# Performance work log

Measured on AMD Instinct MI355X. Metric: run time of the kernel, lower is better.

## Reference

```python
import jax, jax.numpy as jnp
import numpy as np

ALPHA = 0.01
EPS = ALPHA / (1.0 - 2.0 * ALPHA)  # boundary_eps


def setup_inputs() -> dict:
    key = jax.random.key(0)
    ks = jax.random.split(key, 9)
    B, D, K = 32768, 256, 1024
    x = jax.random.normal(ks[0], (B, D), dtype=jnp.float32)
    logp = jnp.zeros((B, 1), dtype=jnp.float32)
    actnorm1_bias = jax.random.normal(ks[1], (D,), dtype=jnp.float32) * 0.1
    actnorm1_weight = jax.random.normal(ks[2], (D,), dtype=jnp.float32) * 0.1
    actnorm2_bias = jax.random.normal(ks[3], (D,), dtype=jnp.float32) * 0.1
    actnorm2_weight = jax.random.normal(ks[4], (D,), dtype=jnp.float32) * 0.1
    shift_coeff = jax.random.normal(ks[5], (D,), dtype=jnp.float32)
    anchor_pts = jax.random.normal(ks[6], (K, D), dtype=jnp.float32)
    mixture_logits = jax.random.normal(ks[7], (K,), dtype=jnp.float32) * 0.1
    u = jax.random.uniform(ks[8], (D,), dtype=jnp.float32)
    box_min = -(u + 1.0) * 2.0  # guarantees box_max > box_min
    box_max = (u + 1.0) * 2.0
    return dict(x=x, logp=logp, actnorm1_bias=actnorm1_bias,
                actnorm1_weight=actnorm1_weight, actnorm2_bias=actnorm2_bias,
                actnorm2_weight=actnorm2_weight, shift_coeff=shift_coeff,
                anchor_pts=anchor_pts, mixture_logits=mixture_logits,
                box_min=box_min, box_max=box_max)


def _voronoi_forward(x, logp, a1b, a1w, a2b, a2w, shift_raw, anchors, mix_logits,
                     box_min, box_max):
    B, D = x.shape
    # actnorm1: y = (x + bias) * exp(weight); logp -= logdet
    x = (x + a1b) * jnp.exp(a1w)
    logp = logp - jnp.sum(a1w)
    # logit_transform.inverse: x = (sigmoid(x) - alpha) / (1 - 2*alpha)
    s = jax.nn.sigmoid(x)
    logdet = jnp.sum(jax.nn.log_sigmoid(x) + jax.nn.log_sigmoid(-x)
                     - jnp.log(1.0 - 2.0 * ALPHA), axis=1, keepdims=True)
    x = (s - ALPHA) / (1.0 - 2.0 * ALPHA)
    logp = logp - logdet
    # rescale from [-eps, 1+eps] to [0, 1]
    lo, hi = -EPS, 1.0 + EPS
    x = (x - lo) / (hi - lo)
    logp = logp - (-jnp.log(hi - lo) * D)
    # box constraints: affine to [box_min, box_max]
    x = x * (box_max - box_min) + box_min
    logp = logp - jnp.sum(jnp.log(box_max - box_min))
    # find_nearest: argmin squared distance over K anchors (GEMM form, no BxKxD tensor)
    d2 = (jnp.sum(x * x, axis=1, keepdims=True)
          - 2.0 * x @ anchors.T
          + jnp.sum(anchors * anchors, axis=1))  # [B, K]
    idx = jnp.argmin(d2, axis=1)  # [B]
    x_k = anchors[idx]  # gather nearest anchor, [B, D]
    # shift toward the nearest anchor
    sc = jax.nn.sigmoid(shift_raw) * 0.98 + 0.01  # (0.01, 0.99)
    x = x + sc * (x_k - x)
    logp = logp - jnp.sum(jnp.log(1.0 - sc))
    # map_outside_cell: identity with zero logdet (see notes)
    # recentre on the chosen anchor
    x = x - x_k
    # actnorm2
    x = (x + a2b) * jnp.exp(a2w)
    logp = logp - jnp.sum(a2w)
    # mixture log-prob gather
    logp_k = jax.nn.log_softmax(mix_logits)[idx][:, None]
    logp = logp - logp_k
    return x, logp, idx


def reference(x, logp, actnorm1_bias, actnorm1_weight, actnorm2_bias,
              actnorm2_weight, shift_coeff, anchor_pts, mixture_logits,
              box_min, box_max):
    return _voronoi_forward(x, logp, actnorm1_bias, actnorm1_weight,
                            actnorm2_bias, actnorm2_weight, shift_coeff,
                            anchor_pts, mixture_logits, box_min, box_max)
```

## Files before the change

### kernel.cpp

```cpp
#include <hip/hip_runtime.h>
#include <math.h>

namespace {
constexpr int Brows = 32768;
constexpr int Dd = 256;
constexpr int Kk = 1024;

constexpr double kAlpha64 = 0.01;
constexpr double kC164 = 1.0 - 2.0 * 0.01;
constexpr double kEps64 = 0.01 / (1.0 - 2.0 * 0.01);
constexpr double kLo64 = -kEps64;
constexpr double kHi64 = 1.0 + kEps64;

constexpr int WS_E1W = 0;
constexpr int WS_WD = 256;
constexpr int WS_P = 512;
constexpr int WS_Q = 768;
constexpr int WS_C = 1024;
constexpr int WS_AA = 1088;
constexpr int WS_LSM = 2112;
}

__global__ void precol_kernel(const float* __restrict__ a1w,
                              const float* __restrict__ a2w,
                              const float* __restrict__ a2b,
                              const float* __restrict__ shiftc,
                              const float* __restrict__ bmin,
                              const float* __restrict__ bmax,
                              float* __restrict__ ws) {
  const int d = threadIdx.x;
  const float w1 = a1w[d], w2 = a2w[d];
  const float wd = __fsub_rn(bmax[d], bmin[d]);
  const float sc = 1.0f / (1.0f + expf(-shiftc[d])) * 0.98f + 0.01f;
  const float e2 = expf(w2);
  ws[WS_E1W + d] = expf(w1);
  ws[WS_WD + d] = wd;
  ws[WS_P + d] = (1.0f - sc) * e2;
  ws[WS_Q + d] = a2b[d] * e2;
  float contrib = -w1 - w2 - logf(wd) - logf(1.0f - sc);
#pragma unroll
  for (int o = 32; o > 0; o >>= 1) contrib += __shfl_xor(contrib, o, 64);
  __shared__ float red[4];
  if ((d & 63) == 0) red[d >> 6] = contrib;
  __syncthreads();
  if (d == 0) {
    float Cv = red[0] + red[1] + red[2] + red[3];
    Cv += (float)Dd * (float)(log(kC164) + log(kHi64 - kLo64));
    ws[WS_C] = Cv;
  }
}

template <typename F>
__device__ inline float pw128_sq(F ld) {
  float r[8];
#pragma unroll
  for (int j = 0; j < 8; ++j) {
    const float v = ld(j);
    r[j] = __fmul_rn(v, v);
  }
  for (int i = 8; i < 128; i += 8) {
#pragma unroll
    for (int j = 0; j < 8; ++j) {
      const float v = ld(i + j);
      r[j] = __fadd_rn(r[j], __fmul_rn(v, v));
    }
  }
  const float s01 = __fadd_rn(r[0], r[1]);
  const float s23 = __fadd_rn(r[2], r[3]);
  const float s45 = __fadd_rn(r[4], r[5]);
  const float s67 = __fadd_rn(r[6], r[7]);
  return __fadd_rn(__fadd_rn(s01, s23), __fadd_rn(s45, s67));
}

__global__ void anorm_kernel(const float* __restrict__ anchors,
                             float* __restrict__ ws) {
  const int k = blockIdx.x * 256 + threadIdx.x;
  const float* a = anchors + (size_t)k * Dd;
  const float b0 = pw128_sq([&](int i) { return a[i]; });
  const float b1 = pw128_sq([&](int i) { return a[128 + i]; });
  ws[WS_AA + k] = __fadd_rn(b0, b1);
}

__global__ void lsm_kernel(const float* __restrict__ logits,
                           float* __restrict__ ws) {
  __shared__ float sm[1024];
  const int t = threadIdx.x;
  const float v = logits[t];
  sm[t] = v;
  __syncthreads();
  for (int o = 512; o > 0; o >>= 1) {
    if (t < o) sm[t] = fmaxf(sm[t], sm[t + o]);
    __syncthreads();
  }
  const float mx = sm[0];
  __syncthreads();
  sm[t] = expf(v - mx);
  __syncthreads();
  for (int o = 512; o > 0; o >>= 1) {
    if (t < o) sm[t] += sm[t + o];
    __syncthreads();
  }
  const float lse = mx + logf(sm[0]);
  ws[WS_LSM + t] = v - lse;
}

__global__ __launch_bounds__(256, 2) void voronoi_main(
    const float* __restrict__ x, const float* __restrict__ logp_in,
    const float* __restrict__ a1b, const float* __restrict__ anchors,
    const float* __restrict__ bmin, const float* __restrict__ ws,
    float* __restrict__ out) {
  __shared__ float xt[Dd][68];
  __shared__ float at[8][256];
  __shared__ float logdet_s[64];
  __shared__ float xx_s[64];
  __shared__ int bidx_s[64];

  const int t = threadIdx.x;
  const int r0 = blockIdx.x * 64;

  const float LOF = (float)kLo64;
  const float HLF = (float)(kHi64 - kLo64);
  const float ALPHAF = (float)kAlpha64;
  const float C1F = (float)kC164;

  {
    const int r = t >> 2, j = t & 3;
    const float* xrow = x + (size_t)(r0 + r) * Dd;
    float ld = 0.0f;
#pragma unroll
    for (int it = 0; it < 16; ++it) {
      const int c = it * 16 + j * 4;
      const float4 xv = *(const float4*)(xrow + c);
      const float4 bv = *(const float4*)(a1b + c);
      const float4 ev = *(const float4*)(ws + WS_E1W + c);
      const float4 wv = *(const float4*)(ws + WS_WD + c);
      const float4 mv = *(const float4*)(bmin + c);
      const float xs[4] = {xv.x, xv.y, xv.z, xv.w};
      const float bs[4] = {bv.x, bv.y, bv.z, bv.w};
      const float es[4] = {ev.x, ev.y, ev.z, ev.w};
      const float wds[4] = {wv.x, wv.y, wv.z, wv.w};
      const float ms[4] = {mv.x, mv.y, mv.z, mv.w};
#pragma unroll
      for (int w = 0; w < 4; ++w) {
        const float y = __fmul_rn(__fadd_rn(xs[w], bs[w]), es[w]);
        const float ay = fabsf(y);
        const float e = expf(-ay);
        ld += -ay - 2.0f * log1pf(e);
        const float den = __fadd_rn(1.0f, e);
        const float s = (y >= 0.0f) ? __fdiv_rn(1.0f, den) : __fdiv_rn(e, den);
        const float x3 = __fdiv_rn(__fsub_rn(s, ALPHAF), C1F);
        const float x4v = __fdiv_rn(__fsub_rn(x3, LOF), HLF);
        const float x5 = __fadd_rn(__fmul_rn(x4v, wds[w]), ms[w]);
        xt[c + w][r] = x5;
      }
    }
    ld += __shfl_xor(ld, 1, 64);
    ld += __shfl_xor(ld, 2, 64);
    if (j == 0) logdet_s[r] = ld;
  }
  __syncthreads();

  if (t < 64) {
    const float b0 = pw128_sq([&](int i) { return xt[i][t]; });
    const float b1 = pw128_sq([&](int i) { return xt[128 + i][t]; });
    xx_s[t] = __fadd_rn(b0, b1);
  }
  __syncthreads();

  const int tc = t & 63;
  const int tr = t >> 6;
  const int tr16 = tr * 16, tc4 = tc * 4;

  float xxr[16];
#pragma unroll
  for (int i = 0; i < 16; ++i) xxr[i] = xx_s[tr16 + i];

  float bd2[16];
  int bidx[16];
#pragma unroll
  for (int i = 0; i < 16; ++i) {
    bd2[i] = 3.0e38f;
    bidx[i] = 0;
  }

  for (int kt = 0; kt < 4; ++kt) {
    float acc[16][4];
#pragma unroll
    for (int i = 0; i < 16; ++i)
#pragma unroll
      for (int j = 0; j < 4; ++j) acc[i][j] = 0.0f;

    for (int dc = 0; dc < 32; ++dc) {
      __syncthreads();
#pragma unroll
      for (int m = 0; m < 2; ++m) {
        const int u = t + m * 256;
        const int k = u >> 1, q = u & 1;
        const float4 av = *(const float4*)(anchors +
                                           (size_t)(kt * 256 + k) * Dd +
                                           dc * 8 + q * 4);
        at[q * 4 + 0][k] = av.x;
        at[q * 4 + 1][k] = av.y;
        at[q * 4 + 2][k] = av.z;
        at[q * 4 + 3][k] = av.w;
      }
      __syncthreads();
#pragma unroll
      for (int dd = 0; dd < 8; ++dd) {
        const int dg = dc * 8 + dd;
        const float4 xf0 = *(const float4*)(&xt[dg][tr16]);
        const float4 xf1 = *(const float4*)(&xt[dg][tr16 + 4]);
        const float4 xf2 = *(const float4*)(&xt[dg][tr16 + 8]);
        const float4 xf3 = *(const float4*)(&xt[dg][tr16 + 12]);
        const float4 af = *(const float4*)(&at[dd][tc4]);
        const float xv[16] = {xf0.x, xf0.y, xf0.z, xf0.w, xf1.x, xf1.y,
                              xf1.z, xf1.w, xf2.x, xf2.y, xf2.z, xf2.w,
                              xf3.x, xf3.y, xf3.z, xf3.w};
#pragma unroll
        for (int i = 0; i < 16; ++i) {
          acc[i][0] = fmaf(xv[i], af.x, acc[i][0]);
          acc[i][1] = fmaf(xv[i], af.y, acc[i][1]);
          acc[i][2] = fmaf(xv[i], af.z, acc[i][2]);
          acc[i][3] = fmaf(xv[i], af.w, acc[i][3]);
        }
      }
    }
#pragma unroll
    for (int j = 0; j < 4; ++j) {
      const int k = kt * 256 + tc4 + j;
      const float aa = ws[WS_AA + k];
#pragma unroll
      for (int i = 0; i < 16; ++i) {
        const float twod = __fadd_rn(acc[i][j], acc[i][j]);
        const float d2 = __fadd_rn(__fsub_rn(xxr[i], twod), aa);
        if (d2 < bd2[i]) {
          bd2[i] = d2;
          bidx[i] = k;
        }
      }
    }
  }
#pragma unroll
  for (int o = 1; o < 64; o <<= 1) {
#pragma unroll
    for (int i = 0; i < 16; ++i) {
      const float od = __shfl_xor(bd2[i], o, 64);
      const int oi = __shfl_xor(bidx[i], o, 64);
      if (od < bd2[i] || (od == bd2[i] && oi < bidx[i])) {
        bd2[i] = od;
        bidx[i] = oi;
      }
    }
  }
  if (tc == 0) {
#pragma unroll
    for (int i = 0; i < 16; ++i) bidx_s[tr16 + i] = bidx[i];
  }
  __syncthreads();

  {
    const int r = t >> 2, j = t & 3;
    const int k = bidx_s[r];
    const float* arow = anchors + (size_t)k * Dd;
    float* orow = out + (size_t)(r0 + r) * Dd;
#pragma unroll
    for (int it = 0; it < 16; ++it) {
      const int c = it * 16 + j * 4;
      const float4 av = *(const float4*)(arow + c);
      const float4 pv = *(const float4*)(ws + WS_P + c);
      const float4 qv = *(const float4*)(ws + WS_Q + c);
      float4 ov;
      ov.x = fmaf(xt[c + 0][r] - av.x, pv.x, qv.x);
      ov.y = fmaf(xt[c + 1][r] - av.y, pv.y, qv.y);
      ov.z = fmaf(xt[c + 2][r] - av.z, pv.z, qv.z);
      ov.w = fmaf(xt[c + 3][r] - av.w, pv.w, qv.w);
      *(float4*)(orow + c) = ov;
    }
  }
  if (t < 64) {
    const int rr = t;
    const int kk2 = bidx_s[rr];
    const float lp =
        logp_in[r0 + rr] + ws[WS_C] - logdet_s[rr] - ws[WS_LSM + kk2];
    out[(size_t)Brows * Dd + r0 + rr] = lp;
    out[(size_t)Brows * Dd + Brows + r0 + rr] = (float)kk2;
  }
}

extern "C" void kernel_launch(void* const* d_in, const int* in_sizes, int n_in,
                              void* d_out, int out_size, void* d_ws,
                              size_t ws_size, hipStream_t stream) {
  const float* x = (const float*)d_in[0];
  const float* logp = (const float*)d_in[1];
  const float* a1b = (const float*)d_in[2];
  const float* a1w = (const float*)d_in[3];
  const float* a2b = (const float*)d_in[4];
  const float* a2w = (const float*)d_in[5];
  const float* shiftc = (const float*)d_in[6];
  const float* anch = (const float*)d_in[7];
  const float* mixl = (const float*)d_in[8];
  const float* bmin = (const float*)d_in[9];
  const float* bmax = (const float*)d_in[10];
  float* ws = (float*)d_ws;
  float* out = (float*)d_out;

  precol_kernel<<<1, 256, 0, stream>>>(a1w, a2w, a2b, shiftc, bmin, bmax, ws);
  anorm_kernel<<<Kk / 256, 256, 0, stream>>>(anch, ws);
  lsm_kernel<<<1, 1024, 0, stream>>>(mixl, ws);
  voronoi_main<<<Brows / 64, 256, 0, stream>>>(x, logp, a1b, anch, bmin, ws,
                                               out);
}
```

Baseline: 379.9 us.

## Split transform into separate kernel and double-buffer anchor tiles in GEMM kernel

Moves the elementwise sigmoid/box transform into its own kernel that writes a transposed x5 matrix, row norms and logdet to workspace. A new 512-thread GEMM kernel processes 128 rows per block, reads x directly from global memory in the transposed layout, and double-buffers anchor tiles in shared memory so the next tile's load overlaps with compute. This aims to cut per-block shared memory and the serialised transform phase to raise occupancy and overlap. In exchange it adds a 32 MB round trip through global memory, uncached-in-LDS x reads in the inner loop, and depends on the workspace being large enough, with the old kernel kept as a fallback.

```diff
diff --git a/kernel.cpp b/kernel.cpp
--- a/kernel.cpp
+++ b/kernel.cpp
@@ -19,6 +19,10 @@
 constexpr int WS_C = 1024;
 constexpr int WS_AA = 1088;
 constexpr int WS_LSM = 2112;
+constexpr int WS_XX = 4096;
+constexpr int WS_LOGDET = 36864;
+constexpr int WS_X5T = 69632;
+constexpr size_t WS_NEED_BYTES = (size_t)(WS_X5T + Dd * Brows) * 4;
 }
 
 __global__ void precol_kernel(const float* __restrict__ a1w,
@@ -104,7 +108,229 @@
   ws[WS_LSM + t] = v - lse;
 }
 
-__global__ __launch_bounds__(256, 2) void voronoi_main(
+__device__ inline void stage1_transform(const float* __restrict__ x,
+                                        const float* __restrict__ a1b,
+                                        const float* __restrict__ bmin,
+                                        const float* __restrict__ ws,
+                                        float (*xt)[68], int t, int r0,
+                                        float* ld_out ) {
+  const float LOF = (float)kLo64;
+  const float HLF = (float)(kHi64 - kLo64);
+  const float ALPHAF = (float)kAlpha64;
+  const float C1F = (float)kC164;
+  const int r = t >> 2, j = t & 3;
+  const float* xrow = x + (size_t)(r0 + r) * Dd;
+  float ld = 0.0f;
+#pragma unroll
+  for (int it = 0; it < 16; ++it) {
+    const int c = it * 16 + j * 4;
+    const float4 xv = *(const float4*)(xrow + c);
+    const float4 bv = *(const float4*)(a1b + c);
+    const float4 ev = *(const float4*)(ws + WS_E1W + c);
+    const float4 wv = *(const float4*)(ws + WS_WD + c);
+    const float4 mv = *(const float4*)(bmin + c);
+    const float xs[4] = {xv.x, xv.y, xv.z, xv.w};
+    const float bs[4] = {bv.x, bv.y, bv.z, bv.w};
+    const float es[4] = {ev.x, ev.y, ev.z, ev.w};
+    const float wds[4] = {wv.x, wv.y, wv.z, wv.w};
+    const float ms[4] = {mv.x, mv.y, mv.z, mv.w};
+#pragma unroll
+    for (int w = 0; w < 4; ++w) {
+      const float y = __fmul_rn(__fadd_rn(xs[w], bs[w]), es[w]);
+      const float ay = fabsf(y);
+      const float e = expf(-ay);
+      ld += -ay - 2.0f * log1pf(e);
+      const float den = __fadd_rn(1.0f, e);
+      const float s = (y >= 0.0f) ? __fdiv_rn(1.0f, den) : __fdiv_rn(e, den);
+      const float x3 = __fdiv_rn(__fsub_rn(s, ALPHAF), C1F);
+      const float x4v = __fdiv_rn(__fsub_rn(x3, LOF), HLF);
+      const float x5 = __fadd_rn(__fmul_rn(x4v, wds[w]), ms[w]);
+      xt[c + w][r] = x5;
+    }
+  }
+  ld += __shfl_xor(ld, 1, 64);
+  ld += __shfl_xor(ld, 2, 64);
+  *ld_out = ld;
+}
+
+__global__ __launch_bounds__(256, 2) void transform_kernel(
+    const float* __restrict__ x, const float* __restrict__ a1b,
+    const float* __restrict__ bmin, float* __restrict__ ws) {
+  __shared__ float xt[Dd][68];
+  const int t = threadIdx.x;
+  const int r0 = blockIdx.x * 64;
+  float ld;
+  stage1_transform(x, a1b, bmin, ws, xt, t, r0, &ld);
+  if ((t & 3) == 0) ws[WS_LOGDET + r0 + (t >> 2)] = ld;
+  __syncthreads();
+  if (t < 64) {
+    const float b0 = pw128_sq([&](int i) { return xt[i][t]; });
+    const float b1 = pw128_sq([&](int i) { return xt[128 + i][t]; });
+    ws[WS_XX + r0 + t] = __fadd_rn(b0, b1);
+  }
+  const int lane = t & 63, wv = t >> 6;
+#pragma unroll 4
+  for (int i = 0; i < 64; ++i) {
+    const int d = wv + i * 4;
+    ws[WS_X5T + (size_t)d * Brows + r0 + lane] = xt[d][lane];
+  }
+}
+
+__global__ __launch_bounds__(512, 4) void voronoi_gemm(
+    const float* __restrict__ logp_in, const float* __restrict__ anchors,
+    const float* __restrict__ ws, float* __restrict__ out) {
+  __shared__ float at[2][8][256];
+  __shared__ float bd2_s[128];
+  __shared__ int bidx_s[128];
+
+  const int t = threadIdx.x;
+  const int r0 = blockIdx.x * 128;
+  const int tc = t & 63;
+  const int tr = t >> 6;
+  const int tr16 = tr * 16, tc4 = tc * 4;
+  const float* __restrict__ x5t = ws + WS_X5T;
+
+  if (t < 128) {
+    bd2_s[t] = 3.0e38f;
+    bidx_s[t] = 0;
+  }
+
+  const int sk = t >> 1, sh = t & 1;
+
+  for (int kt = 0; kt < 4; ++kt) {
+    float acc[16][4];
+#pragma unroll
+    for (int i = 0; i < 16; ++i)
+#pragma unroll
+      for (int j = 0; j < 4; ++j) acc[i][j] = 0.0f;
+
+    const float* abase =
+        anchors + (size_t)(kt * 256 + sk) * Dd + sh * 4;
+    {
+      const float4 av = *(const float4*)(abase);
+      at[0][sh * 4 + 0][sk] = av.x;
+      at[0][sh * 4 + 1][sk] = av.y;
+      at[0][sh * 4 + 2][sk] = av.z;
+      at[0][sh * 4 + 3][sk] = av.w;
+    }
+    __syncthreads();
+
+    for (int dc = 0; dc < 32; ++dc) {
+      const int buf = dc & 1;
+      float4 avn;
+      if (dc < 31) avn = *(const float4*)(abase + (dc + 1) * 8);
+#pragma unroll
+      for (int dd = 0; dd < 8; ++dd) {
+        const int dg = dc * 8 + dd;
+        const float* xp = x5t + (size_t)dg * Brows + r0 + tr16;
+        const float4 xf0 = *(const float4*)(xp);
+        const float4 xf1 = *(const float4*)(xp + 4);
+        const float4 xf2 = *(const float4*)(xp + 8);
+        const float4 xf3 = *(const float4*)(xp + 12);
+        const float4 af = *(const float4*)(&at[buf][dd][tc4]);
+        const float xv[16] = {xf0.x, xf0.y, xf0.z, xf0.w, xf1.x, xf1.y,
+                              xf1.z, xf1.w, xf2.x, xf2.y, xf2.z, xf2.w,
+                              xf3.x, xf3.y, xf3.z, xf3.w};
+#pragma unroll
+        for (int i = 0; i < 16; ++i) {
+          acc[i][0] = fmaf(xv[i], af.x, acc[i][0]);
+          acc[i][1] = fmaf(xv[i], af.y, acc[i][1]);
+          acc[i][2] = fmaf(xv[i], af.z, acc[i][2]);
+          acc[i][3] = fmaf(xv[i], af.w, acc[i][3]);
+        }
+      }
+      if (dc < 31) {
+        __syncthreads();
+        at[buf ^ 1][sh * 4 + 0][sk] = avn.x;
+        at[buf ^ 1][sh * 4 + 1][sk] = avn.y;
+        at[buf ^ 1][sh * 4 + 2][sk] = avn.z;
+        at[buf ^ 1][sh * 4 + 3][sk] = avn.w;
+        __syncthreads();
+      }
+    }
+
+    float bd2[16];
+    int bidx[16];
+#pragma unroll
+    for (int i = 0; i < 16; ++i) {
+      bd2[i] = 3.0e38f;
+      bidx[i] = 0;
+    }
+#pragma unroll
+    for (int j = 0; j < 4; ++j) {
+      const int k = kt * 256 + tc4 + j;
+      const float aa = ws[WS_AA + k];
+#pragma unroll
+      for (int i = 0; i < 16; ++i) {
+        const float xxv = ws[WS_XX + r0 + tr16 + i];
+        const float twod = __fadd_rn(acc[i][j], acc[i][j]);
+        const float d2 = __fadd_rn(__fsub_rn(xxv, twod), aa);
+        if (d2 < bd2[i]) {
+          bd2[i] = d2;
+          bidx[i] = k;
+        }
+      }
+    }
+#pragma unroll
+    for (int o = 1; o < 64; o <<= 1) {
+#pragma unroll
+      for (int i = 0; i < 16; ++i) {
+        const float od = __shfl_xor(bd2[i], o, 64);
+        const int oi = __shfl_xor(bidx[i], o, 64);
+        if (od < bd2[i] || (od == bd2[i] && oi < bidx[i])) {
+          bd2[i] = od;
+          bidx[i] = oi;
+        }
+      }
+    }
+    if (tc == 0) {
+#pragma unroll
+      for (int i = 0; i < 16; ++i) {
+        const int row = tr16 + i;
+        if (bd2[i] < bd2_s[row] ||
+            (bd2[i] == bd2_s[row] && bidx[i] < bidx_s[row])) {
+          bd2_s[row] = bd2[i];
+          bidx_s[row] = bidx[i];
+        }
+      }
+    }
+    __syncthreads();
+  }
+
+  {
+    const int r = t >> 2, j = t & 3;
+    const int k = bidx_s[r];
+    const float* arow = anchors + (size_t)k * Dd;
+    float* orow = out + (size_t)(r0 + r) * Dd;
+#pragma unroll
+    for (int it = 0; it < 16; ++it) {
+      const int c = it * 16 + j * 4;
+      const float4 av = *(const float4*)(arow + c);
+      const float4 pv = *(const float4*)(ws + WS_P + c);
+      const float4 qv = *(const float4*)(ws + WS_Q + c);
+      float x5v[4];
+#pragma unroll
+      for (int w = 0; w < 4; ++w)
+        x5v[w] = x5t[(size_t)(c + w) * Brows + r0 + r];
+      float4 ov;
+      ov.x = fmaf(x5v[0] - av.x, pv.x, qv.x);
+      ov.y = fmaf(x5v[1] - av.y, pv.y, qv.y);
+      ov.z = fmaf(x5v[2] - av.z, pv.z, qv.z);
+      ov.w = fmaf(x5v[3] - av.w, pv.w, qv.w);
+      *(float4*)(orow + c) = ov;
+    }
+  }
+  if (t < 128) {
+    const int rr = t;
+    const int kk2 = bidx_s[rr];
+    const float lp = logp_in[r0 + rr] + ws[WS_C] -
+                     ws[WS_LOGDET + r0 + rr] - ws[WS_LSM + kk2];
+    out[(size_t)Brows * Dd + r0 + rr] = lp;
+    out[(size_t)Brows * Dd + Brows + r0 + rr] = (float)kk2;
+  }
+}
+
+__global__ __launch_bounds__(256, 2) void voronoi_fb(
     const float* __restrict__ x, const float* __restrict__ logp_in,
     const float* __restrict__ a1b, const float* __restrict__ anchors,
     const float* __restrict__ bmin, const float* __restrict__ ws,
@@ -117,49 +343,10 @@
 
   const int t = threadIdx.x;
   const int r0 = blockIdx.x * 64;
-
-  const float LOF = (float)kLo64;
-  const float HLF = (float)(kHi64 - kLo64);
-  const float ALPHAF = (float)kAlpha64;
-  const float C1F = (float)kC164;
-
-  {
-    const int r = t >> 2, j = t & 3;
-    const float* xrow = x + (size_t)(r0 + r) * Dd;
-    float ld = 0.0f;
-#pragma unroll
-    for (int it = 0; it < 16; ++it) {
-      const int c = it * 16 + j * 4;
-      const float4 xv = *(const float4*)(xrow + c);
-      const float4 bv = *(const float4*)(a1b + c);
-      const float4 ev = *(const float4*)(ws + WS_E1W + c);
-      const float4 wv = *(const float4*)(ws + WS_WD + c);
-      const float4 mv = *(const float4*)(bmin + c);
-      const float xs[4] = {xv.x, xv.y, xv.z, xv.w};
-      const float bs[4] = {bv.x, bv.y, bv.z, bv.w};
-      const float es[4] = {ev.x, ev.y, ev.z, ev.w};
-      const float wds[4] = {wv.x, wv.y, wv.z, wv.w};
-      const float ms[4] = {mv.x, mv.y, mv.z, mv.w};
-#pragma unroll
-      for (int w = 0; w < 4; ++w) {
-        const float y = __fmul_rn(__fadd_rn(xs[w], bs[w]), es[w]);
-        const float ay = fabsf(y);
-        const float e = expf(-ay);
-        ld += -ay - 2.0f * log1pf(e);
-        const float den = __fadd_rn(1.0f, e);
-        const float s = (y >= 0.0f) ? __fdiv_rn(1.0f, den) : __fdiv_rn(e, den);
-        const float x3 = __fdiv_rn(__fsub_rn(s, ALPHAF), C1F);
-        const float x4v = __fdiv_rn(__fsub_rn(x3, LOF), HLF);
-        const float x5 = __fadd_rn(__fmul_rn(x4v, wds[w]), ms[w]);
-        xt[c + w][r] = x5;
-      }
-    }
-    ld += __shfl_xor(ld, 1, 64);
-    ld += __shfl_xor(ld, 2, 64);
-    if (j == 0) logdet_s[r] = ld;
-  }
-  __syncthreads();
-
+  float ld;
+  stage1_transform(x, a1b, bmin, ws, xt, t, r0, &ld);
+  if ((t & 3) == 0) logdet_s[t >> 2] = ld;
+  __syncthreads();
   if (t < 64) {
     const float b0 = pw128_sq([&](int i) { return xt[i][t]; });
     const float b1 = pw128_sq([&](int i) { return xt[128 + i][t]; });
@@ -167,14 +354,11 @@
   }
   __syncthreads();
 
-  const int tc = t & 63;
-  const int tr = t >> 6;
+  const int tc = t & 63, tr = t >> 6;
   const int tr16 = tr * 16, tc4 = tc * 4;
-
   float xxr[16];
 #pragma unroll
   for (int i = 0; i < 16; ++i) xxr[i] = xx_s[tr16 + i];
-
   float bd2[16];
   int bidx[16];
 #pragma unroll
@@ -182,14 +366,12 @@
     bd2[i] = 3.0e38f;
     bidx[i] = 0;
   }
-
   for (int kt = 0; kt < 4; ++kt) {
     float acc[16][4];
 #pragma unroll
     for (int i = 0; i < 16; ++i)
 #pragma unroll
       for (int j = 0; j < 4; ++j) acc[i][j] = 0.0f;
-
     for (int dc = 0; dc < 32; ++dc) {
       __syncthreads();
 #pragma unroll
@@ -257,7 +439,6 @@
     for (int i = 0; i < 16; ++i) bidx_s[tr16 + i] = bidx[i];
   }
   __syncthreads();
-
   {
     const int r = t >> 2, j = t & 3;
     const int k = bidx_s[r];
@@ -307,6 +488,11 @@
   precol_kernel<<<1, 256, 0, stream>>>(a1w, a2w, a2b, shiftc, bmin, bmax, ws);
   anorm_kernel<<<Kk / 256, 256, 0, stream>>>(anch, ws);
   lsm_kernel<<<1, 1024, 0, stream>>>(mixl, ws);
-  voronoi_main<<<Brows / 64, 256, 0, stream>>>(x, logp, a1b, anch, bmin, ws,
+  if (ws_size >= WS_NEED_BYTES) {
+    transform_kernel<<<Brows / 64, 256, 0, stream>>>(x, a1b, bmin, ws);
+    voronoi_gemm<<<Brows / 128, 512, 0, stream>>>(logp, anch, ws, out);
+  } else {
+    voronoi_fb<<<Brows / 64, 256, 0, stream>>>(x, logp, a1b, anch, bmin, ws,
                                                out);
-}
+  }
+}
```

Measured after the change: 1.214 ms. 220% more time.

## Widen per-thread anchor tile to 16x8 with split anchor staging buffers

Applied to the files above, without the earlier changes.

Each thread now accumulates 16 rows by 8 anchors instead of 16 by 4, so the K loop runs 2 passes of 512 anchors instead of 4 passes of 256. Anchors are staged through two 4x256 shared buffers, one float4 per thread per buffer, with an index mapping that gives each thread 8 contiguous anchors. The goal is to load each x value from LDS once per 8 FMAs instead of 4, and to halve the K passes over the x tile. In exchange the accumulators double to 128 registers, which may cause spills or lower occupancy under the (256, 2) launch bounds, and there are twice as many barriers in the D loop.

```diff
diff --git a/kernel.cpp b/kernel.cpp
--- a/kernel.cpp
+++ b/kernel.cpp
@@ -110,7 +110,8 @@
     const float* __restrict__ bmin, const float* __restrict__ ws,
     float* __restrict__ out) {
   __shared__ float xt[Dd][68];
-  __shared__ float at[8][256];
+  __shared__ float bufA[4][256];
+  __shared__ float bufB[4][256];
   __shared__ float logdet_s[64];
   __shared__ float xx_s[64];
   __shared__ int bidx_s[64];
@@ -183,51 +184,62 @@
     bidx[i] = 0;
   }
 
-  for (int kt = 0; kt < 4; ++kt) {
-    float acc[16][4];
+  const int kApre = ((t >> 2) * 8) + (t & 3);
+  const int kBpre = kApre + 4;
+
+  for (int kt = 0; kt < 2; ++kt) {
+    float acc[16][8];
 #pragma unroll
     for (int i = 0; i < 16; ++i)
 #pragma unroll
-      for (int j = 0; j < 4; ++j) acc[i][j] = 0.0f;
-
-    for (int dc = 0; dc < 32; ++dc) {
+      for (int j = 0; j < 8; ++j) acc[i][j] = 0.0f;
+
+    const float* aA = anchors + (size_t)(kt * 512 + kApre) * Dd;
+    const float* aB = anchors + (size_t)(kt * 512 + kBpre) * Dd;
+
+    for (int dc = 0; dc < 64; ++dc) {
       __syncthreads();
-#pragma unroll
-      for (int m = 0; m < 2; ++m) {
-        const int u = t + m * 256;
-        const int k = u >> 1, q = u & 1;
-        const float4 av = *(const float4*)(anchors +
-                                           (size_t)(kt * 256 + k) * Dd +
-                                           dc * 8 + q * 4);
-        at[q * 4 + 0][k] = av.x;
-        at[q * 4 + 1][k] = av.y;
-        at[q * 4 + 2][k] = av.z;
-        at[q * 4 + 3][k] = av.w;
+      {
+        const float4 avA = *(const float4*)(aA + dc * 4);
+        const float4 avB = *(const float4*)(aB + dc * 4);
+        bufA[0][t] = avA.x;
+        bufA[1][t] = avA.y;
+        bufA[2][t] = avA.z;
+        bufA[3][t] = avA.w;
+        bufB[0][t] = avB.x;
+        bufB[1][t] = avB.y;
+        bufB[2][t] = avB.z;
+        bufB[3][t] = avB.w;
       }
       __syncthreads();
 #pragma unroll
-      for (int dd = 0; dd < 8; ++dd) {
-        const int dg = dc * 8 + dd;
+      for (int dd = 0; dd < 4; ++dd) {
+        const int dg = dc * 4 + dd;
         const float4 xf0 = *(const float4*)(&xt[dg][tr16]);
         const float4 xf1 = *(const float4*)(&xt[dg][tr16 + 4]);
         const float4 xf2 = *(const float4*)(&xt[dg][tr16 + 8]);
         const float4 xf3 = *(const float4*)(&xt[dg][tr16 + 12]);
-        const float4 af = *(const float4*)(&at[dd][tc4]);
+        const float4 afA = *(const float4*)(&bufA[dd][tc4]);
+        const float4 afB = *(const float4*)(&bufB[dd][tc4]);
         const float xv[16] = {xf0.x, xf0.y, xf0.z, xf0.w, xf1.x, xf1.y,
                               xf1.z, xf1.w, xf2.x, xf2.y, xf2.z, xf2.w,
                               xf3.x, xf3.y, xf3.z, xf3.w};
 #pragma unroll
         for (int i = 0; i < 16; ++i) {
-          acc[i][0] = fmaf(xv[i], af.x, acc[i][0]);
-          acc[i][1] = fmaf(xv[i], af.y, acc[i][1]);
-          acc[i][2] = fmaf(xv[i], af.z, acc[i][2]);
-          acc[i][3] = fmaf(xv[i], af.w, acc[i][3]);
+          acc[i][0] = fmaf(xv[i], afA.x, acc[i][0]);
+          acc[i][1] = fmaf(xv[i], afA.y, acc[i][1]);
+          acc[i][2] = fmaf(xv[i], afA.z, acc[i][2]);
+          acc[i][3] = fmaf(xv[i], afA.w, acc[i][3]);
+          acc[i][4] = fmaf(xv[i], afB.x, acc[i][4]);
+          acc[i][5] = fmaf(xv[i], afB.y, acc[i][5]);
+          acc[i][6] = fmaf(xv[i], afB.z, acc[i][6]);
+          acc[i][7] = fmaf(xv[i], afB.w, acc[i][7]);
         }
       }
     }
 #pragma unroll
-    for (int j = 0; j < 4; ++j) {
-      const int k = kt * 256 + tc4 + j;
+    for (int j = 0; j < 8; ++j) {
+      const int k = kt * 512 + tc * 8 + j;
       const float aa = ws[WS_AA + k];
 #pragma unroll
       for (int i = 0; i < 16; ++i) {
```

After: 382.1 us. No clear change (+0.6%).
